# Kernel tuning notes

Hardware: AMD Instinct MI355X
Metric: run time of the kernel (lower is better)

Reference implementation:

```python
import jax, jax.numpy as jnp
import numpy as np

D_MODEL = 1024
N_HEADS = 16
HEAD_DIM = D_MODEL // N_HEADS
SCALE = float(np.sqrt(HEAD_DIM))
NEG_INF = -1e30


def setup_inputs() -> dict:
    key = jax.random.key(0)
    k1, k2, k3 = jax.random.split(key, 3)
    B, S = 4, 2048
    x = jax.random.normal(k1, (B, S, D_MODEL), dtype=jnp.float32)
    attention_mask = jnp.ones((B, S), dtype=jnp.int32)
    # torch Linear(d, 3d, bias=False): y = x @ W^T; store pre-transposed (d, 3d)
    w_qkv = jax.random.normal(k2, (D_MODEL, 3 * D_MODEL), dtype=jnp.float32) * (1.0 / np.sqrt(D_MODEL))
    w_out = jax.random.normal(k3, (D_MODEL, D_MODEL), dtype=jnp.float32) * (1.0 / np.sqrt(D_MODEL))
    return {"x": x, "attention_mask": attention_mask, "w_qkv": w_qkv, "w_out": w_out}


def reference(x, attention_mask, w_qkv, w_out):
    B, S, _ = x.shape
    qkv = jnp.einsum('bsd,de->bse', x, w_qkv)                     # (B,S,3D)
    qkv = qkv.reshape(B, S, 3, N_HEADS, HEAD_DIM)
    q = qkv[:, :, 0].transpose(0, 2, 1, 3)                        # (B,H,S,hd)
    k = qkv[:, :, 1].transpose(0, 2, 1, 3)
    v = qkv[:, :, 2].transpose(0, 2, 1, 3)

    scores = jnp.einsum('bhqd,bhkd->bhqk', q, k) / SCALE          # (B,H,S,S)
    causal_mask = jnp.triu(jnp.ones((S, S), dtype=bool), k=1)     # True above diag
    scores = jnp.where(causal_mask[None, None], NEG_INF, scores)
    pad_mask = (attention_mask == 0)[:, None, None, :]            # (B,1,1,S)
    scores = jnp.where(pad_mask, NEG_INF, scores)

    attn = jax.nn.softmax(scores, axis=-1)                        # dropout=0 (eval)
    out = jnp.einsum('bhqk,bhkd->bhqd', attn, v)                  # (B,H,S,hd)
    out = out.transpose(0, 2, 1, 3).reshape(B, S, D_MODEL)
    return jnp.einsum('bsd,de->bse', out, w_out)
```

## Files before the change

### kernel.cpp

```cpp
#include <hip/hip_runtime.h>


typedef __attribute__((ext_vector_type(8))) short bf16x8;
typedef __attribute__((ext_vector_type(8))) unsigned short u16x8;
typedef __attribute__((ext_vector_type(4))) unsigned short u16x4;
typedef __attribute__((ext_vector_type(4))) float f32x4;

#define MFMA16 __builtin_amdgcn_mfma_f32_16x16x32_bf16

#define GLDS(gp, lp) __builtin_amdgcn_global_load_lds( \
    (const __attribute__((address_space(1))) unsigned int*)(gp), \
    (__attribute__((address_space(3))) unsigned int*)(lp), 16, 0, 0)

__device__ __forceinline__ unsigned short f2bf(float f) {
    union { float f; unsigned int u; } v; v.f = f;
    unsigned int r = v.u + 0x7fffu + ((v.u >> 16) & 1u);
    return (unsigned short)(r >> 16);
}

__global__ void k_f2b(const float* __restrict__ in, unsigned short* __restrict__ out) {
    size_t i = ((size_t)blockIdx.x * 256 + threadIdx.x) * 8;
    float4 f0 = *(const float4*)(in + i);
    float4 f1 = *(const float4*)(in + i + 4);
    u16x8 v;
    v[0] = f2bf(f0.x); v[1] = f2bf(f0.y); v[2] = f2bf(f0.z); v[3] = f2bf(f0.w);
    v[4] = f2bf(f1.x); v[5] = f2bf(f1.y); v[6] = f2bf(f1.z); v[7] = f2bf(f1.w);
    *(u16x8*)(out + i) = v;
}

__global__ void k_maskb(const int* __restrict__ mask, unsigned short* __restrict__ mb) {
    int i = blockIdx.x * 256 + threadIdx.x;
    mb[i] = mask[i] ? (unsigned short)0x3F80 : (unsigned short)0;
}

__global__ void k_transpose(const float* __restrict__ in,
                            unsigned short* __restrict__ out, int R, int C) {
    __shared__ float tile[32][33];
    int c0 = blockIdx.x * 32, r0 = blockIdx.y * 32;
    int tx = threadIdx.x & 31, ty = threadIdx.x >> 5;
    for (int i = ty; i < 32; i += 8)
        tile[i][tx] = in[(size_t)(r0 + i) * C + (c0 + tx)];
    __syncthreads();
    for (int i = ty; i < 32; i += 8)
        out[(size_t)(c0 + i) * R + (r0 + tx)] = f2bf(tile[tx][i]);
}

template <int MODE>
__global__ __launch_bounds__(256) void k_gemm_bt(
    const unsigned short* __restrict__ Ab,
    const unsigned short* __restrict__ Bt,
    float* __restrict__ Cf,
    unsigned short* __restrict__ qb,
    unsigned short* __restrict__ kb,
    unsigned short* __restrict__ vt,
    const int* __restrict__ mask,
    int N, int K)
{
    __shared__ __align__(16) unsigned short la[128 * 32];
    __shared__ __align__(16) unsigned short lb[128 * 32];
    const int t = threadIdx.x;
    const int m0 = blockIdx.y * 128, n0 = blockIdx.x * 128;
    const int w = t >> 6, lane = t & 63;
    const int wm = (w & 1) * 64, wn = (w >> 1) * 64;
    const int lr = lane & 15, lq = lane >> 4;
    const int rr = t >> 2, cc = (t & 3) * 8;

    f32x4 acc[4][4];
    for (int i = 0; i < 4; ++i)
        for (int j = 0; j < 4; ++j)
            acc[i][j] = (f32x4){0.f, 0.f, 0.f, 0.f};

    for (int k0 = 0; k0 < K; k0 += 32) {
        GLDS(&Ab[(size_t)(m0 +      rr) * K + k0 + cc], &la[ w      * 512]);
        GLDS(&Ab[(size_t)(m0 + 64 + rr) * K + k0 + cc], &la[(4 + w) * 512]);
        GLDS(&Bt[(size_t)(n0 +      rr) * K + k0 + cc], &lb[ w      * 512]);
        GLDS(&Bt[(size_t)(n0 + 64 + rr) * K + k0 + cc], &lb[(4 + w) * 512]);
        __syncthreads();
        bf16x8 af[4], bg[4];
        for (int i = 0; i < 4; ++i) {
            af[i] = *(const bf16x8*)&la[(wm + i * 16 + lr) * 32 + lq * 8];
            bg[i] = *(const bf16x8*)&lb[(wn + i * 16 + lr) * 32 + lq * 8];
        }
        for (int i = 0; i < 4; ++i)
            for (int j = 0; j < 4; ++j)
                acc[i][j] = MFMA16(af[i], bg[j], acc[i][j], 0, 0, 0);
        __syncthreads();
    }

    const float QSCALE = 0.18033688f;
    if (MODE == 0) {
        for (int i = 0; i < 4; ++i)
            for (int j = 0; j < 4; ++j)
                for (int r = 0; r < 4; ++r) {
                    int row = m0 + wm + i * 16 + lq * 4 + r;
                    int col = n0 + wn + j * 16 + lr;
                    Cf[(size_t)row * N + col] = acc[i][j][r];
                }
    } else {
        const int which = n0 >> 10;
        if (which < 2) {
            unsigned short* dst = which ? kb : qb;
            const float sc = which ? 1.0f : QSCALE;
            for (int i = 0; i < 4; ++i)
                for (int j = 0; j < 4; ++j)
                    for (int r = 0; r < 4; ++r) {
                        int row = m0 + wm + i * 16 + lq * 4 + r;
                        int col = n0 + wn + j * 16 + lr;
                        int h = (col >> 6) & 15, d = col & 63;
                        int b = row >> 11, s = row & 2047;
                        dst[((size_t)(b * 16 + h) * 2048 + s) * 64 + d] = f2bf(acc[i][j][r] * sc);
                    }
        } else {
            for (int i = 0; i < 4; ++i) {
                int s0 = m0 + wm + i * 16 + lq * 4;
                int b = s0 >> 11, s = s0 & 2047;
                int4 m4 = *(const int4*)&mask[b * 2048 + s];
                for (int j = 0; j < 4; ++j) {
                    int col = n0 + wn + j * 16 + lr;
                    int h = (col >> 6) & 15, d = col & 63;
                    u16x4 pv;
                    pv[0] = m4.x ? f2bf(acc[i][j][0]) : (unsigned short)0;
                    pv[1] = m4.y ? f2bf(acc[i][j][1]) : (unsigned short)0;
                    pv[2] = m4.z ? f2bf(acc[i][j][2]) : (unsigned short)0;
                    pv[3] = m4.w ? f2bf(acc[i][j][3]) : (unsigned short)0;
                    *(u16x4*)&vt[((size_t)(b * 16 + h) * 64 + d) * 2048 + s] = pv;
                }
            }
        }
    }
}

__global__ __launch_bounds__(256, 4) void k_attn(
    const unsigned short* __restrict__ qb,
    const unsigned short* __restrict__ kb,
    const unsigned short* __restrict__ vt,
    const unsigned short* __restrict__ maskbg,
    unsigned short* __restrict__ ao)
{
    __shared__ __align__(16) unsigned short kt_lds[2][64 * 64];
    __shared__ __align__(16) unsigned short vt_lds[2][64 * 64];
    __shared__ __align__(16) unsigned short plds[4][32 * 72];

    const int t = threadIdx.x;
    const int w = t >> 6, lane = t & 63;
    const int lr = lane & 15, lq = lane >> 4;
    const int lr7 = lr & 7;
    const int bh = blockIdx.y, b = bh >> 4, h = bh & 15;

    const unsigned short* qp = qb + (size_t)bh * 2048 * 64;
    const unsigned short* kp = kb + (size_t)bh * 2048 * 64;
    const unsigned short* vp = vt + (size_t)bh * 64 * 2048;
    const unsigned short* mbg = maskbg + b * 2048;
    unsigned short* pw = plds[w];

    const int rowb = lane >> 3, c8 = lane & 7;
    const int sc8 = (c8 ^ rowb) * 8;

    auto stage = [&](int c) {
        const int buf = c & 1;
        const int k0 = c * 64;
        #pragma unroll
        for (int r = 0; r < 2; ++r) {
            const int rg = 8 * (w + 4 * r);
            const int row = rg + rowb;
            GLDS(&kp[(size_t)(k0 + row) * 64 + sc8], &kt_lds[buf][rg * 64]);
            GLDS(&vp[(size_t)row * 2048 + k0 + sc8], &vt_lds[buf][rg * 64]);
        }
    };

    for (int pass = 0; pass < 2; ++pass) {
        const int stripe = pass ? (15 - (int)blockIdx.x) : (int)blockIdx.x;
        const int q0w = stripe * 128 + w * 32;

        bf16x8 aq[2][2];
        #pragma unroll
        for (int qt = 0; qt < 2; ++qt) {
            aq[qt][0] = *(const bf16x8*)&qp[(q0w + qt * 16 + lr) * 64 + lq * 8];
            aq[qt][1] = *(const bf16x8*)&qp[(q0w + qt * 16 + lr) * 64 + 32 + lq * 8];
        }

        f32x4 acc[2][4], lacc[2];
        #pragma unroll
        for (int qt = 0; qt < 2; ++qt) {
            lacc[qt] = (f32x4){0.f, 0.f, 0.f, 0.f};
            for (int j = 0; j < 4; ++j) acc[qt][j] = (f32x4){0.f, 0.f, 0.f, 0.f};
        }

        const int nch = 2 * (stripe + 1);
        stage(0);
        for (int c = 0; c < nch; ++c) {
            __syncthreads();
            if (c + 1 < nch) stage(c + 1);
            const int k0 = c * 64;
            if (k0 < q0w + 32) {
                const unsigned short* kt = kt_lds[c & 1];
                const unsigned short* vtl = vt_lds[c & 1];
                const bool causal = (k0 + 63 > q0w);
                const int kcol0 = (lq ^ lr7) * 8;
                const int kcol1 = ((4 + lq) ^ lr7) * 8;
                #pragma unroll
                for (int ki = 0; ki < 4; ++ki) {
                    bf16x8 kf0 = *(const bf16x8*)&kt[(ki * 16 + lr) * 64 + kcol0];
                    bf16x8 kf1 = *(const bf16x8*)&kt[(ki * 16 + lr) * 64 + kcol1];
                    #pragma unroll
                    for (int qt = 0; qt < 2; ++qt) {
                        f32x4 s = (f32x4){0.f, 0.f, 0.f, 0.f};
                        s = MFMA16(kf0, aq[qt][0], s, 0, 0, 0);
                        s = MFMA16(kf1, aq[qt][1], s, 0, 0, 0);
                        unsigned int u[4];
                        #pragma unroll
                        for (int r = 0; r < 4; ++r) {
                            float scv = s[r];
                            if (causal) {
                                int key = k0 + ki * 16 + lq * 4 + r;
                                int qq  = q0w + qt * 16 + lr;
                                scv = (key <= qq) ? scv : -3.0e38f;
                            }
                            float p = __builtin_amdgcn_exp2f(scv);
                            union { float f; unsigned int u; } cv; cv.f = p;
                            u[r] = cv.u + 0x8000u;
                        }
                        uint2 pk;
                        pk.x = (u[0] >> 16) | (u[1] & 0xffff0000u);
                        pk.y = (u[2] >> 16) | (u[3] & 0xffff0000u);
                        *(uint2*)&pw[(qt * 16 + lr) * 72 + ki * 16 + lq * 4] = pk;
                    }
                }
                #pragma unroll
                for (int kc = 0; kc < 64; kc += 32) {
                    bf16x8 pf0 = *(const bf16x8*)&pw[lr * 72 + kc + lq * 8];
                    bf16x8 pf1 = *(const bf16x8*)&pw[(16 + lr) * 72 + kc + lq * 8];
                    bf16x8 mb  = *(const bf16x8*)&mbg[k0 + kc + lq * 8];
                    const int vcol = (((kc >> 3) + lq) ^ lr7) * 8;
                    #pragma unroll
                    for (int j = 0; j < 4; ++j) {
                        bf16x8 vf = *(const bf16x8*)&vtl[(j * 16 + lr) * 64 + vcol];
                        acc[0][j] = MFMA16(pf0, vf, acc[0][j], 0, 0, 0);
                        acc[1][j] = MFMA16(pf1, vf, acc[1][j], 0, 0, 0);
                    }
                    lacc[0] = MFMA16(pf0, mb, lacc[0], 0, 0, 0);
                    lacc[1] = MFMA16(pf1, mb, lacc[1], 0, 0, 0);
                }
            }
        }

        #pragma unroll
        for (int qt = 0; qt < 2; ++qt) {
            #pragma unroll
            for (int r = 0; r < 4; ++r) {
                float inv = 1.0f / fmaxf(lacc[qt][r], 1e-30f);
                int row = q0w + qt * 16 + lq * 4 + r;
                #pragma unroll
                for (int j = 0; j < 4; ++j) {
                    int d = j * 16 + lr;
                    ao[(size_t)(b * 2048 + row) * 1024 + h * 64 + d] = f2bf(acc[qt][j][r] * inv);
                }
            }
        }
        __syncthreads();
    }
}

extern "C" void kernel_launch(void* const* d_in, const int* in_sizes, int n_in,
                              void* d_out, int out_size, void* d_ws, size_t ws_size,
                              hipStream_t stream)
{
    const float* x    = (const float*)d_in[0];
    const int*   mask = (const int*)d_in[1];
    const float* wqkv = (const float*)d_in[2];
    const float* wout = (const float*)d_in[3];
    float* out = (float*)d_out;

    const size_t NEED = ((size_t)8192 * 1024 + (size_t)3072 * 1024 + (size_t)1024 * 1024 +
                         3 * (size_t)64 * 2048 * 64 + (size_t)8192 * 1024 + 8192) * 2;
    if (ws_size < NEED) return;

    char* ws = (char*)d_ws;
    unsigned short* xb  = (unsigned short*)ws; ws += (size_t)8192 * 1024 * 2;
    unsigned short* w1t = (unsigned short*)ws; ws += (size_t)3072 * 1024 * 2;
    unsigned short* w2t = (unsigned short*)ws; ws += (size_t)1024 * 1024 * 2;
    unsigned short* qb  = (unsigned short*)ws; ws += (size_t)64 * 2048 * 64 * 2;
    unsigned short* kb  = (unsigned short*)ws; ws += (size_t)64 * 2048 * 64 * 2;
    unsigned short* vt  = (unsigned short*)ws; ws += (size_t)64 * 64 * 2048 * 2;
    unsigned short* ao  = (unsigned short*)ws; ws += (size_t)8192 * 1024 * 2;
    unsigned short* mbg = (unsigned short*)ws; ws += (size_t)8192 * 2;

    k_f2b<<<dim3(4096), 256, 0, stream>>>(x, xb);
    k_maskb<<<dim3(32), 256, 0, stream>>>(mask, mbg);
    k_transpose<<<dim3(96, 32), 256, 0, stream>>>(wqkv, w1t, 1024, 3072);
    k_transpose<<<dim3(32, 32), 256, 0, stream>>>(wout, w2t, 1024, 1024);
    k_gemm_bt<1><<<dim3(24, 64), 256, 0, stream>>>(xb, w1t, nullptr, qb, kb, vt, mask, 3072, 1024);
    k_attn<<<dim3(8, 64), 256, 0, stream>>>(qb, kb, vt, mbg, ao);
    k_gemm_bt<0><<<dim3(8, 64), 256, 0, stream>>>(ao, w2t, out, nullptr, nullptr, nullptr, nullptr, 1024, 1024);
}
```

Baseline: 288.8 us.

## Merge prep kernels, one attention stripe per block, use perm packing

```diff
diff --git a/kernel.cpp b/kernel.cpp
--- a/kernel.cpp
+++ b/kernel.cpp
@@ -18,7 +18,8 @@
     return (unsigned short)(r >> 16);
 }
 
-__global__ void k_f2b(const float* __restrict__ in, unsigned short* __restrict__ out) {
+__global__ void k_prep(const float* __restrict__ in, unsigned short* __restrict__ out,
+                       const int* __restrict__ mask, unsigned short* __restrict__ mb) {
     size_t i = ((size_t)blockIdx.x * 256 + threadIdx.x) * 8;
     float4 f0 = *(const float4*)(in + i);
     float4 f1 = *(const float4*)(in + i + 4);
@@ -26,23 +27,27 @@
     v[0] = f2bf(f0.x); v[1] = f2bf(f0.y); v[2] = f2bf(f0.z); v[3] = f2bf(f0.w);
     v[4] = f2bf(f1.x); v[5] = f2bf(f1.y); v[6] = f2bf(f1.z); v[7] = f2bf(f1.w);
     *(u16x8*)(out + i) = v;
-}
-
-__global__ void k_maskb(const int* __restrict__ mask, unsigned short* __restrict__ mb) {
-    int i = blockIdx.x * 256 + threadIdx.x;
-    mb[i] = mask[i] ? (unsigned short)0x3F80 : (unsigned short)0;
-}
-
-__global__ void k_transpose(const float* __restrict__ in,
-                            unsigned short* __restrict__ out, int R, int C) {
+    if (blockIdx.x < 32) {
+        int j = blockIdx.x * 256 + threadIdx.x;
+        mb[j] = mask[j] ? (unsigned short)0x3F80 : (unsigned short)0;
+    }
+}
+
+__global__ void k_transpose2(const float* __restrict__ wqkv, unsigned short* __restrict__ w1t,
+                             const float* __restrict__ wout, unsigned short* __restrict__ w2t) {
     __shared__ float tile[32][33];
-    int c0 = blockIdx.x * 32, r0 = blockIdx.y * 32;
+    const int bx = blockIdx.x;
+    const float* in = (bx < 96) ? wqkv : wout;
+    unsigned short* out = (bx < 96) ? w1t : w2t;
+    const int C = (bx < 96) ? 3072 : 1024;
+    const int c0 = ((bx < 96) ? bx : bx - 96) * 32;
+    const int r0 = blockIdx.y * 32;
     int tx = threadIdx.x & 31, ty = threadIdx.x >> 5;
     for (int i = ty; i < 32; i += 8)
         tile[i][tx] = in[(size_t)(r0 + i) * C + (c0 + tx)];
     __syncthreads();
     for (int i = ty; i < 32; i += 8)
-        out[(size_t)(c0 + i) * R + (r0 + tx)] = f2bf(tile[tx][i]);
+        out[(size_t)(c0 + i) * 1024 + (r0 + tx)] = f2bf(tile[tx][i]);
 }
 
 template <int MODE>
@@ -168,96 +173,93 @@
         }
     };
 
-    for (int pass = 0; pass < 2; ++pass) {
-        const int stripe = pass ? (15 - (int)blockIdx.x) : (int)blockIdx.x;
-        const int q0w = stripe * 128 + w * 32;
-
-        bf16x8 aq[2][2];
-        #pragma unroll
-        for (int qt = 0; qt < 2; ++qt) {
-            aq[qt][0] = *(const bf16x8*)&qp[(q0w + qt * 16 + lr) * 64 + lq * 8];
-            aq[qt][1] = *(const bf16x8*)&qp[(q0w + qt * 16 + lr) * 64 + 32 + lq * 8];
-        }
-
-        f32x4 acc[2][4], lacc[2];
-        #pragma unroll
-        for (int qt = 0; qt < 2; ++qt) {
-            lacc[qt] = (f32x4){0.f, 0.f, 0.f, 0.f};
-            for (int j = 0; j < 4; ++j) acc[qt][j] = (f32x4){0.f, 0.f, 0.f, 0.f};
-        }
-
-        const int nch = 2 * (stripe + 1);
-        stage(0);
-        for (int c = 0; c < nch; ++c) {
-            __syncthreads();
-            if (c + 1 < nch) stage(c + 1);
-            const int k0 = c * 64;
-            if (k0 < q0w + 32) {
-                const unsigned short* kt = kt_lds[c & 1];
-                const unsigned short* vtl = vt_lds[c & 1];
-                const bool causal = (k0 + 63 > q0w);
-                const int kcol0 = (lq ^ lr7) * 8;
-                const int kcol1 = ((4 + lq) ^ lr7) * 8;
+    const int stripe = 15 - (int)blockIdx.x;
+    const int q0w = stripe * 128 + w * 32;
+
+    bf16x8 aq[2][2];
+    #pragma unroll
+    for (int qt = 0; qt < 2; ++qt) {
+        aq[qt][0] = *(const bf16x8*)&qp[(q0w + qt * 16 + lr) * 64 + lq * 8];
+        aq[qt][1] = *(const bf16x8*)&qp[(q0w + qt * 16 + lr) * 64 + 32 + lq * 8];
+    }
+
+    f32x4 acc[2][4], lacc[2];
+    #pragma unroll
+    for (int qt = 0; qt < 2; ++qt) {
+        lacc[qt] = (f32x4){0.f, 0.f, 0.f, 0.f};
+        for (int j = 0; j < 4; ++j) acc[qt][j] = (f32x4){0.f, 0.f, 0.f, 0.f};
+    }
+
+    const int nch = 2 * (stripe + 1);
+    stage(0);
+    for (int c = 0; c < nch; ++c) {
+        __syncthreads();
+        if (c + 1 < nch) stage(c + 1);
+        const int k0 = c * 64;
+        if (k0 < q0w + 32) {
+            const unsigned short* kt = kt_lds[c & 1];
+            const unsigned short* vtl = vt_lds[c & 1];
+            const bool causal = (k0 + 63 > q0w);
+            const int kcol0 = (lq ^ lr7) * 8;
+            const int kcol1 = ((4 + lq) ^ lr7) * 8;
+            #pragma unroll
+            for (int ki = 0; ki < 4; ++ki) {
+                bf16x8 kf0 = *(const bf16x8*)&kt[(ki * 16 + lr) * 64 + kcol0];
+                bf16x8 kf1 = *(const bf16x8*)&kt[(ki * 16 + lr) * 64 + kcol1];
                 #pragma unroll
-                for (int ki = 0; ki < 4; ++ki) {
-                    bf16x8 kf0 = *(const bf16x8*)&kt[(ki * 16 + lr) * 64 + kcol0];
-                    bf16x8 kf1 = *(const bf16x8*)&kt[(ki * 16 + lr) * 64 + kcol1];
+                for (int qt = 0; qt < 2; ++qt) {
+                    f32x4 s = (f32x4){0.f, 0.f, 0.f, 0.f};
+                    s = MFMA16(kf0, aq[qt][0], s, 0, 0, 0);
+                    s = MFMA16(kf1, aq[qt][1], s, 0, 0, 0);
+                    unsigned int u[4];
                     #pragma unroll
-                    for (int qt = 0; qt < 2; ++qt) {
-                        f32x4 s = (f32x4){0.f, 0.f, 0.f, 0.f};
-                        s = MFMA16(kf0, aq[qt][0], s, 0, 0, 0);
-                        s = MFMA16(kf1, aq[qt][1], s, 0, 0, 0);
-                        unsigned int u[4];
-                        #pragma unroll
-                        for (int r = 0; r < 4; ++r) {
-                            float scv = s[r];
-                            if (causal) {
-                                int key = k0 + ki * 16 + lq * 4 + r;
-                                int qq  = q0w + qt * 16 + lr;
-                                scv = (key <= qq) ? scv : -3.0e38f;
-                            }
-                            float p = __builtin_amdgcn_exp2f(scv);
-                            union { float f; unsigned int u; } cv; cv.f = p;
-                            u[r] = cv.u + 0x8000u;
+                    for (int r = 0; r < 4; ++r) {
+                        float scv = s[r];
+                        if (causal) {
+                            int key = k0 + ki * 16 + lq * 4 + r;
+                            int qq  = q0w + qt * 16 + lr;
+                            scv = (key <= qq) ? scv : -3.0e38f;
                         }
-                        uint2 pk;
-                        pk.x = (u[0] >> 16) | (u[1] & 0xffff0000u);
-                        pk.y = (u[2] >> 16) | (u[3] & 0xffff0000u);
-                        *(uint2*)&pw[(qt * 16 + lr) * 72 + ki * 16 + lq * 4] = pk;
+                        float p = __builtin_amdgcn_exp2f(scv);
+                        union { float f; unsigned int u; } cv; cv.f = p;
+                        u[r] = cv.u;
                     }
-                }
-                #pragma unroll
-                for (int kc = 0; kc < 64; kc += 32) {
-                    bf16x8 pf0 = *(const bf16x8*)&pw[lr * 72 + kc + lq * 8];
-                    bf16x8 pf1 = *(const bf16x8*)&pw[(16 + lr) * 72 + kc + lq * 8];
-                    bf16x8 mb  = *(const bf16x8*)&mbg[k0 + kc + lq * 8];
-                    const int vcol = (((kc >> 3) + lq) ^ lr7) * 8;
-                    #pragma unroll
-                    for (int j = 0; j < 4; ++j) {
-                        bf16x8 vf = *(const bf16x8*)&vtl[(j * 16 + lr) * 64 + vcol];
-                        acc[0][j] = MFMA16(pf0, vf, acc[0][j], 0, 0, 0);
-                        acc[1][j] = MFMA16(pf1, vf, acc[1][j], 0, 0, 0);
-                    }
-                    lacc[0] = MFMA16(pf0, mb, lacc[0], 0, 0, 0);
-                    lacc[1] = MFMA16(pf1, mb, lacc[1], 0, 0, 0);
-                }
-            }
-        }
-
-        #pragma unroll
-        for (int qt = 0; qt < 2; ++qt) {
+                    uint2 pk;
+                    pk.x = __builtin_amdgcn_perm(u[1], u[0], 0x07060302u);
+                    pk.y = __builtin_amdgcn_perm(u[3], u[2], 0x07060302u);
+                    *(uint2*)&pw[(qt * 16 + lr) * 72 + ki * 16 + lq * 4] = pk;
+                }
+            }
             #pragma unroll
-            for (int r = 0; r < 4; ++r) {
-                float inv = 1.0f / fmaxf(lacc[qt][r], 1e-30f);
-                int row = q0w + qt * 16 + lq * 4 + r;
+            for (int kc = 0; kc < 64; kc += 32) {
+                bf16x8 pf0 = *(const bf16x8*)&pw[lr * 72 + kc + lq * 8];
+                bf16x8 pf1 = *(const bf16x8*)&pw[(16 + lr) * 72 + kc + lq * 8];
+                bf16x8 mb  = *(const bf16x8*)&mbg[k0 + kc + lq * 8];
+                const int vcol = (((kc >> 3) + lq) ^ lr7) * 8;
                 #pragma unroll
                 for (int j = 0; j < 4; ++j) {
-                    int d = j * 16 + lr;
-                    ao[(size_t)(b * 2048 + row) * 1024 + h * 64 + d] = f2bf(acc[qt][j][r] * inv);
-                }
-            }
-        }
-        __syncthreads();
+                    bf16x8 vf = *(const bf16x8*)&vtl[(j * 16 + lr) * 64 + vcol];
+                    acc[0][j] = MFMA16(pf0, vf, acc[0][j], 0, 0, 0);
+                    acc[1][j] = MFMA16(pf1, vf, acc[1][j], 0, 0, 0);
+                }
+                lacc[0] = MFMA16(pf0, mb, lacc[0], 0, 0, 0);
+                lacc[1] = MFMA16(pf1, mb, lacc[1], 0, 0, 0);
+            }
+        }
+    }
+
+    #pragma unroll
+    for (int qt = 0; qt < 2; ++qt) {
+        #pragma unroll
+        for (int r = 0; r < 4; ++r) {
+            float inv = 1.0f / fmaxf(lacc[qt][r], 1e-30f);
+            int row = q0w + qt * 16 + lq * 4 + r;
+            #pragma unroll
+            for (int j = 0; j < 4; ++j) {
+                int d = j * 16 + lr;
+                ao[(size_t)(b * 2048 + row) * 1024 + h * 64 + d] = f2bf(acc[qt][j][r] * inv);
+            }
+        }
     }
 }
 
@@ -285,11 +287,9 @@
     unsigned short* ao  = (unsigned short*)ws; ws += (size_t)8192 * 1024 * 2;
     unsigned short* mbg = (unsigned short*)ws; ws += (size_t)8192 * 2;
 
-    k_f2b<<<dim3(4096), 256, 0, stream>>>(x, xb);
-    k_maskb<<<dim3(32), 256, 0, stream>>>(mask, mbg);
-    k_transpose<<<dim3(96, 32), 256, 0, stream>>>(wqkv, w1t, 1024, 3072);
-    k_transpose<<<dim3(32, 32), 256, 0, stream>>>(wout, w2t, 1024, 1024);
+    k_prep<<<dim3(4096), 256, 0, stream>>>(x, xb, mask, mbg);
+    k_transpose2<<<dim3(128, 32), 256, 0, stream>>>(wqkv, w1t, wout, w2t);
     k_gemm_bt<1><<<dim3(24, 64), 256, 0, stream>>>(xb, w1t, nullptr, qb, kb, vt, mask, 3072, 1024);
-    k_attn<<<dim3(8, 64), 256, 0, stream>>>(qb, kb, vt, mbg, ao);
+    k_attn<<<dim3(16, 64), 256, 0, stream>>>(qb, kb, vt, mbg, ao);
     k_gemm_bt<0><<<dim3(8, 64), 256, 0, stream>>>(ao, w2t, out, nullptr, nullptr, nullptr, nullptr, 1024, 1024);
 }
```

Result: slower. 324.8 us (+12.5%).
